# Optimization experiments

Hardware: AMD Instinct MI355X
Metric: run time of the kernel (lower is better)

## Reference

```python
import jax, jax.numpy as jnp
import numpy as np

D_EMB = 256


def setup_inputs() -> dict:
    key = jax.random.key(0)
    ks = jax.random.split(key, 7)
    B, S, d = 4, 4096, D_EMB
    scale = 1.0 / np.sqrt(d)
    return {
        "x": jax.random.normal(ks[0], (B, S, d), jnp.float32),
        "Wqkv": jax.random.normal(ks[1], (d, 3 * d), jnp.float32) * scale,
        "bqkv": jax.random.normal(ks[2], (3 * d,), jnp.float32) * 0.02,
        "Wproj": jax.random.normal(ks[3], (d, d), jnp.float32) * scale,
        "bproj": jax.random.normal(ks[4], (d,), jnp.float32) * 0.02,
        "Wfc": jax.random.normal(ks[5], (d, 1), jnp.float32) * scale,
        "bfc": jax.random.normal(ks[6], (1,), jnp.float32) * 0.02,
    }


def reference(x, Wqkv, bqkv, Wproj, bproj, Wfc, bfc):
    # qkv projection: [B,S,3d] -> split into q,k,v [B,S,d]
    qkv = x @ Wqkv + bqkv
    q, k, v = jnp.split(qkv, 3, axis=2)
    # full attention scores [B,S,S]; note: original applies NO 1/sqrt(d)
    # scaling (dead branch in source), 'traditional' softmax over last dim
    attn_scores = jnp.einsum("bqd,bkd->bqk", q, k)
    attn_weights = jax.nn.softmax(attn_scores, axis=-1)
    y = jnp.einsum("bqk,bkd->bqd", attn_weights, v)
    y = y @ Wproj + bproj
    out = y @ Wfc + bfc  # [B,S,1]
    return out
```

## Files before the change

kernel.cpp:

```cpp
#include <hip/hip_runtime.h>
#include <hip/hip_bf16.h>

#define BQ 4
#define SQ 4096
#define DQ 256
#define N3 768
#define KBLK 64
#define NITER (SQ / KBLK)
#define KHALF (NITER / 2)
#define LOG2E 1.44269504f
#define THR2 11.5415603f

typedef __attribute__((ext_vector_type(8))) _Float16 f16x8;
typedef __attribute__((ext_vector_type(4))) float f32x4;
typedef __attribute__((ext_vector_type(4))) unsigned int u32x4;

__device__ __forceinline__ short f2h(float f) {
  _Float16 h = (_Float16)f;
  union { _Float16 h; short s; } v; v.h = h;
  return v.s;
}

__device__ __forceinline__ void gload16(const void* g, void* lds) {
  __builtin_amdgcn_global_load_lds(
      (const __attribute__((address_space(1))) unsigned int*)g,
      (__attribute__((address_space(3))) unsigned int*)lds, 16, 0, 0);
}

__global__ __launch_bounds__(256) void prep_kernel(
    const float* __restrict__ Wqkv, const float* __restrict__ Wproj,
    const float* __restrict__ bproj, const float* __restrict__ Wfc,
    const float* __restrict__ bfc, short* __restrict__ W16T,
    float* __restrict__ Wc) {
  const int t = threadIdx.x;
  if (blockIdx.x == 48) {
    __shared__ float wf[256];
    wf[t] = Wfc[t];
    __syncthreads();
    float acc = 0.f;
    for (int j = 0; j < 256; ++j) acc += Wproj[(size_t)t * 256 + j] * wf[j];
    Wc[t] = acc;
    if (t == 0) {
      float c = bfc[0];
      for (int j = 0; j < 256; ++j) c += bproj[j] * wf[j];
      Wc[256] = c;
    }
    return;
  }
  __shared__ float tile[64][65];
  const int nb = (blockIdx.x % 12) * 64;
  const int kb = (blockIdx.x / 12) * 64;
  const int tr = t >> 6, tc = t & 63;
#pragma unroll
  for (int i = 0; i < 16; ++i)
    tile[tr + i * 4][tc] = Wqkv[(size_t)(kb + tr + i * 4) * N3 + nb + tc];
  __syncthreads();
#pragma unroll
  for (int i = 0; i < 16; ++i)
    W16T[(size_t)(nb + tr + i * 4) * 256 + kb + tc] = f2h(tile[tc][tr + i * 4]);
}

__global__ __launch_bounds__(1024, 4) void qkv_kernel(
    const float* __restrict__ x, const short* __restrict__ W16T,
    const float* __restrict__ bqkv, const float* __restrict__ Wc,
    short* __restrict__ Qb, short* __restrict__ Kb, float* __restrict__ u) {
  __shared__ short xs[64][264];
  __shared__ short ws[2][64][256];
  __shared__ float u_red[4][4][16];
  const int t = threadIdx.x;
  const int l = t & 63, w = t >> 6;
  const int lr = l & 15, lg = l >> 4;
  const int mq = w >> 2, nq = w & 3;
  const int Mbase = blockIdx.x * 64;

#define STAGE_W(BUF, NT)                                                      \
  {                                                                           \
    _Pragma("unroll") for (int i = 0; i < 2; ++i) {                           \
      const int n = w * 4 + i * 2 + (l >> 5);                                 \
      const int gc = (l & 31) ^ (n & 7);                                      \
      gload16(W16T + (size_t)((NT)*64 + n) * 256 + gc * 8,                    \
              &ws[BUF][w * 4 + i * 2][0]);                                    \
    }                                                                         \
  }

  STAGE_W(0, 0);

  {
    const int m = t >> 4, kc = (t & 15) * 16;
    const float* src = x + (size_t)(Mbase + m) * DQ + kc;
    short tmp[16];
#pragma unroll
    for (int i = 0; i < 16; ++i) tmp[i] = f2h(src[i]);
    *(u32x4*)&xs[m][kc] = *(u32x4*)&tmp[0];
    *(u32x4*)&xs[m][kc + 8] = *(u32x4*)&tmp[8];
  }

  float bias_qk[8], bias_u[4], wc_u[4];
#pragma unroll
  for (int i = 0; i < 8; ++i) bias_qk[i] = bqkv[i * 64 + nq * 16 + lr];
#pragma unroll
  for (int i = 0; i < 4; ++i) {
    bias_u[i] = bqkv[512 + i * 64 + nq * 16 + lr];
    wc_u[i] = Wc[i * 64 + nq * 16 + lr];
  }

  __syncthreads();

  unsigned qksto[8][2];
  float upart[4] = {0.f, 0.f, 0.f, 0.f};

#pragma unroll
  for (int nt = 0; nt < 12; ++nt) {
    const int cur = nt & 1;
    if (nt + 1 < 12) {
      STAGE_W(cur ^ 1, nt + 1);
      asm volatile("s_waitcnt vmcnt(2)" ::: "memory");
    } else {
      asm volatile("s_waitcnt vmcnt(0)" ::: "memory");
    }
    __builtin_amdgcn_s_barrier();
    __builtin_amdgcn_sched_barrier(0);

    f32x4 acc = {};
    const char* wR = (const char*)&ws[cur][nq * 16 + lr][0];
#pragma unroll
    for (int kk = 0; kk < 8; ++kk) {
      f16x8 af = *(f16x8*)&xs[mq * 16 + lr][kk * 32 + lg * 8];
      f16x8 bfr = *(const f16x8*)(wR + (((4 * kk + lg) ^ (lr & 7)) << 4));
      acc = __builtin_amdgcn_mfma_f32_16x16x32_f16(af, bfr, acc, 0, 0, 0);
    }
    if (nt < 8) {
      const float sc = (nt < 4) ? 1.f : LOG2E;
      unsigned s0 = (unsigned short)f2h((acc[0] + bias_qk[nt]) * sc);
      unsigned s1 = (unsigned short)f2h((acc[1] + bias_qk[nt]) * sc);
      unsigned s2 = (unsigned short)f2h((acc[2] + bias_qk[nt]) * sc);
      unsigned s3 = (unsigned short)f2h((acc[3] + bias_qk[nt]) * sc);
      qksto[nt][0] = s0 | (s1 << 16);
      qksto[nt][1] = s2 | (s3 << 16);
    } else {
#pragma unroll
      for (int r = 0; r < 4; ++r) upart[r] += (acc[r] + bias_u[nt - 8]) * wc_u[nt - 8];
    }
    __builtin_amdgcn_s_barrier();
  }

#pragma unroll
  for (int nt = 0; nt < 8; ++nt) {
    const int col = nt * 64 + nq * 16 + lr;
#pragma unroll
    for (int r = 0; r < 4; ++r) {
      const int row = Mbase + mq * 16 + lg * 4 + r;
      const short sv = (short)((qksto[nt][r >> 1] >> ((r & 1) * 16)) & 0xFFFF);
      if (col < 256) Qb[(size_t)row * DQ + col] = sv;
      else           Kb[(size_t)row * DQ + (col - 256)] = sv;
    }
  }

#pragma unroll
  for (int mask = 1; mask <= 8; mask <<= 1)
#pragma unroll
    for (int r = 0; r < 4; ++r) upart[r] += __shfl_xor(upart[r], mask, 64);
  if (lr == 0) {
#pragma unroll
    for (int r = 0; r < 4; ++r) u_red[mq][nq][lg * 4 + r] = upart[r];
  }
  __syncthreads();
  if (t < 64)
    u[Mbase + t] = u_red[t >> 4][0][t & 15] + u_red[t >> 4][1][t & 15] +
                   u_red[t >> 4][2][t & 15] + u_red[t >> 4][3][t & 15];
#undef STAGE_W
}

__global__ __launch_bounds__(256, 2) void attn_kernel(
    const short* __restrict__ Qb, const short* __restrict__ Kb,
    const float* __restrict__ u, float* __restrict__ Pm,
    float* __restrict__ Pd, float* __restrict__ Pn) {
  __shared__ short Ks[2][64][256];
  __shared__ __align__(16) float u_lds[2048];
  __shared__ float Mrg[4][64][3];

  const int t = threadIdx.x;
  const int l = t & 63, w = t >> 6;
  const int lr = l & 15, lg = l >> 4;
  const int bid = blockIdx.x;
  const int b = bid & 3;
  const int half = (bid >> 2) & 1;
  const int qbase = (bid >> 3) * 64;

  const short* kbase = Kb + ((size_t)b * SQ + (size_t)half * (SQ / 2)) * DQ;
  const float* ubase = u + (size_t)b * SQ + half * (SQ / 2);

#define STAGE(BUF, KB)                                                      \
  {                                                                         \
    _Pragma("unroll") for (int i = 0; i < 8; ++i) {                         \
      const int kr = w * 16 + i * 2 + (l >> 5);                             \
      const int gc = (l & 31) ^ (kr & 7);                                   \
      gload16(kbase + (size_t)((KB)*64 + kr) * DQ + gc * 8,                 \
              &Ks[BUF][w * 16 + i * 2][0]);                                 \
    }                                                                       \
  }

  {
    const short* qsrc = Qb + (size_t)(b * SQ + qbase) * DQ;
#pragma unroll
    for (int i = 0; i < 8; ++i) {
      const int qr = w * 16 + i * 2 + (l >> 5);
      const int gc = (l & 31) ^ (qr & 7);
      gload16(qsrc + (size_t)qr * DQ + gc * 8, &Ks[0][w * 16 + i * 2][0]);
    }
  }
  gload16(ubase + w * 256 + (l << 2), &u_lds[w * 256]);
  gload16(ubase + (4 + w) * 256 + (l << 2), &u_lds[(4 + w) * 256]);

  int koff[8];
#pragma unroll
  for (int kk = 0; kk < 8; ++kk) koff[kk] = ((4 * kk + lg) ^ (lr & 7)) << 4;

  asm volatile("s_waitcnt vmcnt(0)" ::: "memory");
  __syncthreads();

  f16x8 qf[4][8];
#pragma unroll
  for (int mm = 0; mm < 4; ++mm) {
    const char* qR = (const char*)&Ks[0][mm * 16 + lr][0];
#pragma unroll
    for (int kk = 0; kk < 8; ++kk)
      qf[mm][kk] = *(const f16x8*)(qR + koff[kk]);
  }
  __syncthreads();

  float m_run[4] = {-1e30f, -1e30f, -1e30f, -1e30f};
  float num[4] = {}, den[4] = {};

  STAGE(0, 0);

  for (int kb = 0; kb < KHALF; ++kb) {
    const int cur = kb & 1;
    asm volatile("s_waitcnt vmcnt(0)" ::: "memory");
    __builtin_amdgcn_s_barrier();
    __builtin_amdgcn_sched_barrier(0);
    if (kb + 1 < KHALF) STAGE(cur ^ 1, kb + 1);

    const char* kR = (const char*)&Ks[cur][w * 16 + lr][0];
    f32x4 s[4] = {};
    __builtin_amdgcn_s_setprio(1);
#pragma unroll
    for (int kk = 0; kk < 8; ++kk) {
      f16x8 kf = *(const f16x8*)(kR + koff[kk]);
      s[0] = __builtin_amdgcn_mfma_f32_16x16x32_f16(kf, qf[0][kk], s[0], 0, 0, 0);
      s[1] = __builtin_amdgcn_mfma_f32_16x16x32_f16(kf, qf[1][kk], s[1], 0, 0, 0);
      s[2] = __builtin_amdgcn_mfma_f32_16x16x32_f16(kf, qf[2][kk], s[2], 0, 0, 0);
      s[3] = __builtin_amdgcn_mfma_f32_16x16x32_f16(kf, qf[3][kk], s[3], 0, 0, 0);
    }
    __builtin_amdgcn_s_setprio(0);

    float mx[4];
#pragma unroll
    for (int mm = 0; mm < 4; ++mm)
      mx[mm] = fmaxf(fmaxf(s[mm][0], s[mm][1]), fmaxf(s[mm][2], s[mm][3]));
    const bool over = (mx[0] > m_run[0] + THR2) || (mx[1] > m_run[1] + THR2) ||
                      (mx[2] > m_run[2] + THR2) || (mx[3] > m_run[3] + THR2);
    if (__any(over)) {
#pragma unroll
      for (int mm = 0; mm < 4; ++mm) {
        float mt = mx[mm];
        mt = fmaxf(mt, __shfl_xor(mt, 16, 64));
        mt = fmaxf(mt, __shfl_xor(mt, 32, 64));
        const float mn = fmaxf(m_run[mm], mt);
        const float sc = __builtin_amdgcn_exp2f(m_run[mm] - mn);
        m_run[mm] = mn;
        num[mm] *= sc;
        den[mm] *= sc;
      }
    }
    {
      const f32x4 uv = *(const f32x4*)&u_lds[kb * 64 + w * 16 + lg * 4];
#pragma unroll
      for (int mm = 0; mm < 4; ++mm)
#pragma unroll
        for (int r = 0; r < 4; ++r) {
          const float p = __builtin_amdgcn_exp2f(s[mm][r] - m_run[mm]);
          den[mm] += p;
          num[mm] += p * uv[r];
        }
    }
  }

#pragma unroll
  for (int mm = 0; mm < 4; ++mm) {
    num[mm] += __shfl_xor(num[mm], 16, 64);
    num[mm] += __shfl_xor(num[mm], 32, 64);
    den[mm] += __shfl_xor(den[mm], 16, 64);
    den[mm] += __shfl_xor(den[mm], 32, 64);
  }
  if (lg == 0) {
#pragma unroll
    for (int mm = 0; mm < 4; ++mm) {
      Mrg[w][mm * 16 + lr][0] = m_run[mm];
      Mrg[w][mm * 16 + lr][1] = den[mm];
      Mrg[w][mm * 16 + lr][2] = num[mm];
    }
  }
  __syncthreads();

  if (t < 64) {
    float M = Mrg[0][t][0];
#pragma unroll
    for (int hh = 1; hh < 4; ++hh) M = fmaxf(M, Mrg[hh][t][0]);
    float dt = 0.f, nt = 0.f;
#pragma unroll
    for (int hh = 0; hh < 4; ++hh) {
      const float e = __builtin_amdgcn_exp2f(Mrg[hh][t][0] - M);
      dt += e * Mrg[hh][t][1];
      nt += e * Mrg[hh][t][2];
    }
    const size_t idx = (size_t)half * (BQ * SQ) + (size_t)b * SQ + qbase + t;
    Pm[idx] = M; Pd[idx] = dt; Pn[idx] = nt;
  }
#undef STAGE
}

__global__ void merge_kernel(const float* __restrict__ Pm,
                             const float* __restrict__ Pd,
                             const float* __restrict__ Pn,
                             const float* __restrict__ Wc,
                             float* __restrict__ out) {
  const int gid = blockIdx.x * 256 + threadIdx.x;
  const float m0 = Pm[gid], m1 = Pm[BQ * SQ + gid];
  const float M = fmaxf(m0, m1);
  const float e0 = __builtin_amdgcn_exp2f(m0 - M);
  const float e1 = __builtin_amdgcn_exp2f(m1 - M);
  const float den = e0 * Pd[gid] + e1 * Pd[BQ * SQ + gid];
  const float num = e0 * Pn[gid] + e1 * Pn[BQ * SQ + gid];
  out[gid] = num / den + Wc[256];
}

extern "C" void kernel_launch(void* const* d_in, const int* in_sizes, int n_in,
                              void* d_out, int out_size, void* d_ws, size_t ws_size,
                              hipStream_t stream) {
  const float* x     = (const float*)d_in[0];
  const float* Wqkv  = (const float*)d_in[1];
  const float* bqkv  = (const float*)d_in[2];
  const float* Wproj = (const float*)d_in[3];
  const float* bproj = (const float*)d_in[4];
  const float* Wfc   = (const float*)d_in[5];
  const float* bfc   = (const float*)d_in[6];
  float* out = (float*)d_out;

  const size_t SEG = (size_t)BQ * SQ * DQ * 2;
  char* wsb = (char*)d_ws;
  short* Qb   = (short*)(wsb);
  short* Kb   = (short*)(wsb + SEG);
  char* base  = wsb + 2 * SEG;
  float* Wc   = (float*)(base);
  float* u    = (float*)(base + 4096);
  short* W16T = (short*)(base + 4096 + 65536);
  float* Pm   = (float*)(base + 4096 + 65536 + 393216);
  float* Pd   = Pm + 2 * BQ * SQ;
  float* Pn   = Pd + 2 * BQ * SQ;

  prep_kernel<<<49, 256, 0, stream>>>(Wqkv, Wproj, bproj, Wfc, bfc, W16T, Wc);
  qkv_kernel<<<256, 1024, 0, stream>>>(x, W16T, bqkv, Wc, Qb, Kb, u);
  attn_kernel<<<512, 256, 0, stream>>>(Qb, Kb, u, Pm, Pd, Pn);
  merge_kernel<<<BQ * SQ / 256, 256, 0, stream>>>(Pm, Pd, Pn, Wc, out);
}
```

Before: 93.32 us.

## Accumulate softmax numerator and denominator with an MFMA instead of VALU reductions

The per-key sums of p*u and p are now computed by packing the probabilities to fp16 and running a 16x16x16 MFMA against a small matrix whose rows hold u, ones, and zeros. This removes the scalar FMA accumulation and the cross-lane shuffle reduction at the end. The u vector is stored in fp16 to fit the MFMA operand format, which halves its staging load. In exchange, probabilities and u lose precision (round-toward-zero fp16), and most of the MFMA output is wasted.

```diff
diff --git a/kernel.cpp b/kernel.cpp
--- a/kernel.cpp
+++ b/kernel.cpp
@@ -12,6 +12,7 @@
 #define THR2 11.5415603f
 
 typedef __attribute__((ext_vector_type(8))) _Float16 f16x8;
+typedef __attribute__((ext_vector_type(4))) _Float16 f16x4;
 typedef __attribute__((ext_vector_type(4))) float f32x4;
 typedef __attribute__((ext_vector_type(4))) unsigned int u32x4;
 
@@ -63,7 +64,7 @@
 __global__ __launch_bounds__(1024, 4) void qkv_kernel(
     const float* __restrict__ x, const short* __restrict__ W16T,
     const float* __restrict__ bqkv, const float* __restrict__ Wc,
-    short* __restrict__ Qb, short* __restrict__ Kb, float* __restrict__ u) {
+    short* __restrict__ Qb, short* __restrict__ Kb, short* __restrict__ u16) {
   __shared__ short xs[64][264];
   __shared__ short ws[2][64][256];
   __shared__ float u_red[4][4][16];
@@ -166,17 +167,17 @@
   }
   __syncthreads();
   if (t < 64)
-    u[Mbase + t] = u_red[t >> 4][0][t & 15] + u_red[t >> 4][1][t & 15] +
-                   u_red[t >> 4][2][t & 15] + u_red[t >> 4][3][t & 15];
+    u16[Mbase + t] = f2h(u_red[t >> 4][0][t & 15] + u_red[t >> 4][1][t & 15] +
+                         u_red[t >> 4][2][t & 15] + u_red[t >> 4][3][t & 15]);
 #undef STAGE_W
 }
 
 __global__ __launch_bounds__(256, 2) void attn_kernel(
     const short* __restrict__ Qb, const short* __restrict__ Kb,
-    const float* __restrict__ u, float* __restrict__ Pm,
+    const short* __restrict__ u16, float* __restrict__ Pm,
     float* __restrict__ Pd, float* __restrict__ Pn) {
   __shared__ short Ks[2][64][256];
-  __shared__ __align__(16) float u_lds[2048];
+  __shared__ __align__(16) short u_lds[2048];
   __shared__ float Mrg[4][64][3];
 
   const int t = threadIdx.x;
@@ -188,7 +189,7 @@
   const int qbase = (bid >> 3) * 64;
 
   const short* kbase = Kb + ((size_t)b * SQ + (size_t)half * (SQ / 2)) * DQ;
-  const float* ubase = u + (size_t)b * SQ + half * (SQ / 2);
+  const short* ubase = u16 + (size_t)b * SQ + half * (SQ / 2);
 
 #define STAGE(BUF, KB)                                                      \
   {                                                                         \
@@ -209,8 +210,7 @@
       gload16(qsrc + (size_t)qr * DQ + gc * 8, &Ks[0][w * 16 + i * 2][0]);
     }
   }
-  gload16(ubase + w * 256 + (l << 2), &u_lds[w * 256]);
-  gload16(ubase + (4 + w) * 256 + (l << 2), &u_lds[(4 + w) * 256]);
+  gload16(ubase + w * 512 + (l << 3), &u_lds[w * 512]);
 
   int koff[8];
 #pragma unroll
@@ -230,7 +230,7 @@
   __syncthreads();
 
   float m_run[4] = {-1e30f, -1e30f, -1e30f, -1e30f};
-  float num[4] = {}, den[4] = {};
+  f32x4 numden[4] = {};
 
   STAGE(0, 0);
 
@@ -269,36 +269,41 @@
         const float mn = fmaxf(m_run[mm], mt);
         const float sc = __builtin_amdgcn_exp2f(m_run[mm] - mn);
         m_run[mm] = mn;
-        num[mm] *= sc;
-        den[mm] *= sc;
+#pragma unroll
+        for (int r = 0; r < 4; ++r) numden[mm][r] *= sc;
       }
     }
+
+    f16x4 uf;
     {
-      const f32x4 uv = *(const f32x4*)&u_lds[kb * 64 + w * 16 + lg * 4];
-#pragma unroll
-      for (int mm = 0; mm < 4; ++mm)
-#pragma unroll
-        for (int r = 0; r < 4; ++r) {
-          const float p = __builtin_amdgcn_exp2f(s[mm][r] - m_run[mm]);
-          den[mm] += p;
-          num[mm] += p * uv[r];
-        }
-    }
-  }
-
-#pragma unroll
-  for (int mm = 0; mm < 4; ++mm) {
-    num[mm] += __shfl_xor(num[mm], 16, 64);
-    num[mm] += __shfl_xor(num[mm], 32, 64);
-    den[mm] += __shfl_xor(den[mm], 16, 64);
-    den[mm] += __shfl_xor(den[mm], 32, 64);
-  }
+      const f16x4 uraw = *(const f16x4*)&u_lds[kb * 64 + w * 16 + lg * 4];
+#pragma unroll
+      for (int j = 0; j < 4; ++j)
+        uf[j] = (lr == 0) ? uraw[j]
+                          : ((lr == 1) ? (_Float16)1.0f : (_Float16)0.0f);
+    }
+
+#pragma unroll
+    for (int mm = 0; mm < 4; ++mm) {
+      const float p0 = __builtin_amdgcn_exp2f(s[mm][0] - m_run[mm]);
+      const float p1 = __builtin_amdgcn_exp2f(s[mm][1] - m_run[mm]);
+      const float p2 = __builtin_amdgcn_exp2f(s[mm][2] - m_run[mm]);
+      const float p3 = __builtin_amdgcn_exp2f(s[mm][3] - m_run[mm]);
+      const auto lo = __builtin_amdgcn_cvt_pkrtz(p0, p1);
+      const auto hi = __builtin_amdgcn_cvt_pkrtz(p2, p3);
+      f16x4 pf;
+      pf[0] = (_Float16)lo[0]; pf[1] = (_Float16)lo[1];
+      pf[2] = (_Float16)hi[0]; pf[3] = (_Float16)hi[1];
+      numden[mm] = __builtin_amdgcn_mfma_f32_16x16x16f16(uf, pf, numden[mm], 0, 0, 0);
+    }
+  }
+
   if (lg == 0) {
 #pragma unroll
     for (int mm = 0; mm < 4; ++mm) {
       Mrg[w][mm * 16 + lr][0] = m_run[mm];
-      Mrg[w][mm * 16 + lr][1] = den[mm];
-      Mrg[w][mm * 16 + lr][2] = num[mm];
+      Mrg[w][mm * 16 + lr][1] = numden[mm][1];
+      Mrg[w][mm * 16 + lr][2] = numden[mm][0];
     }
   }
   __syncthreads();
@@ -353,14 +358,14 @@
   short* Kb   = (short*)(wsb + SEG);
   char* base  = wsb + 2 * SEG;
   float* Wc   = (float*)(base);
-  float* u    = (float*)(base + 4096);
+  short* u16  = (short*)(base + 4096);
   short* W16T = (short*)(base + 4096 + 65536);
   float* Pm   = (float*)(base + 4096 + 65536 + 393216);
   float* Pd   = Pm + 2 * BQ * SQ;
   float* Pn   = Pd + 2 * BQ * SQ;
 
   prep_kernel<<<49, 256, 0, stream>>>(Wqkv, Wproj, bproj, Wfc, bfc, W16T, Wc);
-  qkv_kernel<<<256, 1024, 0, stream>>>(x, W16T, bqkv, Wc, Qb, Kb, u);
-  attn_kernel<<<512, 256, 0, stream>>>(Qb, Kb, u, Pm, Pd, Pn);
+  qkv_kernel<<<256, 1024, 0, stream>>>(x, W16T, bqkv, Wc, Qb, Kb, u16);
+  attn_kernel<<<512, 256, 0, stream>>>(Qb, Kb, u16, Pm, Pd, Pn);
   merge_kernel<<<BQ * SQ / 256, 256, 0, stream>>>(Pm, Pd, Pn, Wc, out);
 }
```

Result: no change. 92.65 us (-0.7%).
